# Kernel tuning notes

Measured on AMD Instinct MI355X. Metric: run time of the kernel, lower is better.

## Reference

```python
import jax, jax.numpy as jnp
import numpy as np

B, S, F, H = 16, 2048, 1024, 16
D = F // H
EPS = 1e-5


def setup_inputs() -> dict:
    key = jax.random.key(0)
    ks = jax.random.split(key, 10)
    scale = 1.0 / np.sqrt(F)
    return {
        "x": jax.random.normal(ks[0], (B, S, F), jnp.float32),
        "Wq": jax.random.normal(ks[1], (F, F), jnp.float32) * scale,
        "bq": jnp.zeros((F,), jnp.float32),
        "Wk": jax.random.normal(ks[2], (F, F), jnp.float32) * scale,
        "bk": jnp.zeros((F,), jnp.float32),
        "Wv": jax.random.normal(ks[3], (F, F), jnp.float32) * scale,
        "bv": jnp.zeros((F,), jnp.float32),
        "Wo": jax.random.normal(ks[4], (F, F), jnp.float32) * scale,
        "bo": jnp.zeros((F,), jnp.float32),
        "gamma": jnp.ones((F,), jnp.float32),
        "beta": jnp.zeros((F,), jnp.float32),
    }


def reference(x, Wq, bq, Wk, bk, Wv, bv, Wo, bo, gamma, beta):
    # x: (B, S, F). Dropout is identity in eval mode.
    b, s, f = x.shape
    q = (x @ Wq + bq).reshape(b, s, H, D)
    k = (x @ Wk + bk).reshape(b, s, H, D)
    v = (x @ Wv + bv).reshape(b, s, H, D)
    # Faithful to source: the einsum (applied to permuted tensors) contracts
    # across HEADS at each sequence position -> scores (B, S, H, H).
    energy = jnp.einsum('bshd,bsgd->bshg', q, k) / (D ** 0.5)
    attn = jax.nn.softmax(energy, axis=-1)  # softmax over key-head axis
    out = jnp.einsum('bshg,bsgd->bshd', attn, v).reshape(b, s, f)
    out = out @ Wo + bo
    # LayerNorm over last dim (eps=1e-5, affine)
    mu = jnp.mean(out, axis=-1, keepdims=True)
    var = jnp.mean((out - mu) ** 2, axis=-1, keepdims=True)
    return (out - mu) * jax.lax.rsqrt(var + EPS) * gamma + beta
```

## Files before the change

### kernel.cpp

```cpp
#include <hip/hip_runtime.h>
#include <hip/hip_bf16.h>
#include <stdint.h>

#define MM   32768
#define FFD  1024
#define NQKV 3072

typedef __bf16 bf16x8 __attribute__((ext_vector_type(8)));
typedef float  f32x4  __attribute__((ext_vector_type(4)));

__device__ __forceinline__ unsigned short f2bf_bits(float f){
  __hip_bfloat16 h = __float2bfloat16(f);
  unsigned short u;
  __builtin_memcpy(&u, &h, 2);
  return u;
}

__device__ __forceinline__ void gld16(const void* g, void* l){
  const unsigned int* gu = (const unsigned int*)g;
  unsigned int* lu = (unsigned int*)l;
  __builtin_amdgcn_global_load_lds(
      (const __attribute__((address_space(1))) unsigned int*)gu,
      (__attribute__((address_space(3))) unsigned int*)lu,
      16, 0, 0);
}

#define BARRIER() do { asm volatile("" ::: "memory"); \
                       __builtin_amdgcn_s_barrier();  \
                       asm volatile("" ::: "memory"); } while(0)

__global__ __launch_bounds__(256) void k_convert_bf16(const float* __restrict__ in,
                                                      unsigned short* __restrict__ out,
                                                      int n4){
  int i = blockIdx.x * 256 + threadIdx.x;
  if (i >= n4) return;
  float4 v = ((const float4*)in)[i];
  ushort4 r;
  r.x = f2bf_bits(v.x); r.y = f2bf_bits(v.y);
  r.z = f2bf_bits(v.z); r.w = f2bf_bits(v.w);
  ((ushort4*)out)[i] = r;
}

__global__ __launch_bounds__(256) void k_transpose_bf16(const float* __restrict__ in,
                                                        unsigned short* __restrict__ out,
                                                        int rows, int cols){
  __shared__ float tile[32][33];
  int bc = blockIdx.x * 32, br = blockIdx.y * 32;
  int tx = threadIdx.x, ty = threadIdx.y;
  #pragma unroll
  for (int j = 0; j < 32; j += 8)
    tile[ty + j][tx] = in[(size_t)(br + ty + j) * cols + bc + tx];
  __syncthreads();
  #pragma unroll
  for (int j = 0; j < 32; j += 8)
    out[(size_t)(bc + ty + j) * rows + br + tx] = f2bf_bits(tile[tx][ty + j]);
}

template <bool BF16OUT>
__global__ __launch_bounds__(512, 2) void k_gemm_bt(
    const unsigned short* __restrict__ A,
    const unsigned short* __restrict__ Bt,
    const float* __restrict__ b0, const float* __restrict__ b1, const float* __restrict__ b2,
    void* __restrict__ Cout, int M, int N, int K)
{
  __shared__ alignas(16) char smem[131072];

  const int tid  = threadIdx.x;
  const int lane = tid & 63;
  const int wave = tid >> 6;
  const int wr = wave >> 2, wc = wave & 3;
  const int quad = lane >> 4, lrow = lane & 15;
  const int sa = ((lrow >> 1) & 3) << 4;

  const int nwgx = gridDim.x;
  int nwg = nwgx * gridDim.y;
  int bid = blockIdx.y * nwgx + blockIdx.x;
  int cpx = nwg >> 3;
  int nid = (bid & 7) * cpx + (bid >> 3);
  int by = nid / nwgx;
  int bx = nid - by * nwgx;

  const long rowBase = (long)by * 256;
  const long colBase = (long)bx * 256;

  f32x4 acc[8][4];
  #pragma unroll
  for (int i = 0; i < 8; i++)
    #pragma unroll
    for (int j = 0; j < 4; j++)
      acc[i][j] = (f32x4){0.f, 0.f, 0.f, 0.f};

  const int swz8 = 8 * ((tid & 3) ^ ((tid >> 3) & 3));
  const unsigned short* gA = A  + (rowBase + (tid >> 2)) * (long)K + swz8;
  const unsigned short* gB = Bt + (colBase + (tid >> 2)) * (long)K + swz8;
  const long hstep = 128L * K;

  const int nk = K >> 5;

  #pragma unroll
  for (int tt = 0; tt < 3; ++tt){
    char* nb = smem + tt * 32768;
    gld16(gA + tt * 32,         nb +         tid * 16);
    gld16(gA + tt * 32 + hstep, nb +  8192 + tid * 16);
    gld16(gB + tt * 32,         nb + 16384 + tid * 16);
    gld16(gB + tt * 32 + hstep, nb + 24576 + tid * 16);
  }
  asm volatile("s_waitcnt vmcnt(8)" ::: "memory");
  BARRIER();

  for (int t = 0; t < nk; ++t){
    char* buf = smem + (t & 3) * 32768;
    char* nb  = smem + ((t + 3) & 3) * 32768;
    const unsigned short* sA = gA + (long)(t + 3) * 32;
    const unsigned short* sB = gB + (long)(t + 3) * 32;
    const bool st = (t < nk - 3);

    bf16x8 bfr[4];
    #pragma unroll
    for (int p = 0; p < 2; ++p){
      bf16x8 af[4];
      const char* ab = buf + wr * 8192 + p * 4096 + lrow * 64 + ((quad * 16) ^ sa);
      #pragma unroll
      for (int f = 0; f < 4; ++f)
        af[f] = *(const bf16x8*)(ab + f * 1024);
      if (p == 0){
        const char* bb = buf + 16384 + wc * 4096 + lrow * 64 + ((quad * 16) ^ sa);
        #pragma unroll
        for (int n = 0; n < 4; ++n)
          bfr[n] = *(const bf16x8*)(bb + n * 1024);
        if (st){
          gld16(sA,         nb +        tid * 16);
          gld16(sA + hstep, nb + 8192 + tid * 16);
        }
      } else {
        if (st){
          gld16(sB,         nb + 16384 + tid * 16);
          gld16(sB + hstep, nb + 24576 + tid * 16);
        }
      }
      BARRIER();
      __builtin_amdgcn_s_setprio(1);
      #pragma unroll
      for (int f = 0; f < 4; ++f)
        #pragma unroll
        for (int n = 0; n < 4; ++n)
          acc[p * 4 + f][n] =
              __builtin_amdgcn_mfma_f32_16x16x32_bf16(af[f], bfr[n], acc[p * 4 + f][n], 0, 0, 0);
      __builtin_amdgcn_s_setprio(0);
      if (p == 1){
        if (st)               asm volatile("s_waitcnt vmcnt(8)" ::: "memory");
        else if (t == nk - 3) asm volatile("s_waitcnt vmcnt(4)" ::: "memory");
        else if (t == nk - 2) asm volatile("s_waitcnt vmcnt(0)" ::: "memory");
      }
      BARRIER();
    }
  }

  #pragma unroll
  for (int n = 0; n < 4; ++n){
    long col = colBase + wc * 64 + n * 16 + lrow;
    const float* bp = (col < 1024) ? b0 : ((col < 2048) ? b1 : b2);
    float bias = bp[col & 1023];
    #pragma unroll
    for (int m = 0; m < 8; ++m){
      long row0 = rowBase + wr * 128 + (m >> 2) * 64 + (m & 3) * 16 + quad * 4;
      #pragma unroll
      for (int r = 0; r < 4; ++r){
        float v = acc[m][n][r] + bias;
        if constexpr (BF16OUT)
          ((unsigned short*)Cout)[(row0 + r) * (long)N + col] = f2bf_bits(v);
        else
          ((float*)Cout)[(row0 + r) * (long)N + col] = v;
      }
    }
  }
}

__global__ __launch_bounds__(256) void k_attention(const unsigned short* __restrict__ qkv,
                                                   unsigned short* __restrict__ aout){
  constexpr int QOFF = 0;
  constexpr int KOFF = 1152;
  constexpr int VOFF = 2304;
  constexpr int POFF = 4864;
  constexpr int PER  = 5504;
  __shared__ unsigned short smem[4 * PER];

  const int lane = threadIdx.x & 63;
  const int wave = threadIdx.x >> 6;
  const int pos  = blockIdx.x * 4 + wave;
  const int quad = lane >> 4, lidx = lane & 15;

  unsigned short* base = smem + wave * PER;
  unsigned short* Qb = base + QOFF;
  unsigned short* Kb = base + KOFF;
  unsigned short* Vt = base + VOFF;
  unsigned short* Pb = base + POFF;

  {
    uint4 z = {0u, 0u, 0u, 0u};
    *(uint4*)(Vt + lane * 40 + 16) = z;
    *(uint4*)(Vt + lane * 40 + 24) = z;
    *(uint2*)(Pb + (lane >> 2) * 40 + 16 + (lane & 3) * 4) = make_uint2(0u, 0u);
  }

  const unsigned short* src = qkv + (size_t)pos * 3072;
  #pragma unroll
  for (int i = 0; i < 6; i++){
    int c = i * 64 + lane;
    uint4 u = *(const uint4*)(src + c * 8);
    if (i < 4){
      unsigned short* mb = (c < 128) ? Qb : Kb;
      int cc = c & 127;
      *(uint4*)(mb + (cc >> 3) * 72 + (cc & 7) * 8) = u;
    } else {
      int cv = c - 256;
      int g = cv >> 3, d0 = (cv & 7) * 8;
      const unsigned short* us = (const unsigned short*)&u;
      #pragma unroll
      for (int t = 0; t < 8; t++) Vt[(d0 + t) * 40 + g] = us[t];
    }
  }
  __syncthreads();

  f32x4 s = (f32x4){0.f, 0.f, 0.f, 0.f};
  #pragma unroll
  for (int kk = 0; kk < 2; kk++){
    bf16x8 a = *(const bf16x8*)(Qb + lidx * 72 + kk * 32 + quad * 8);
    bf16x8 b = *(const bf16x8*)(Kb + lidx * 72 + kk * 32 + quad * 8);
    s = __builtin_amdgcn_mfma_f32_16x16x32_bf16(a, b, s, 0, 0, 0);
  }

  #pragma unroll
  for (int r = 0; r < 4; r++){
    float v = s[r] * 0.125f;
    float m = v;
    m = fmaxf(m, __shfl_xor(m, 1));
    m = fmaxf(m, __shfl_xor(m, 2));
    m = fmaxf(m, __shfl_xor(m, 4));
    m = fmaxf(m, __shfl_xor(m, 8));
    float e = __expf(v - m);
    float sum = e;
    sum += __shfl_xor(sum, 1);
    sum += __shfl_xor(sum, 2);
    sum += __shfl_xor(sum, 4);
    sum += __shfl_xor(sum, 8);
    float p = e / sum;
    Pb[(quad * 4 + r) * 40 + lidx] = f2bf_bits(p);
  }
  __syncthreads();

  f32x4 o[4];
  #pragma unroll
  for (int n4 = 0; n4 < 4; n4++){
    bf16x8 a = *(const bf16x8*)(Pb + lidx * 40 + quad * 8);
    bf16x8 b = *(const bf16x8*)(Vt + (n4 * 16 + lidx) * 40 + quad * 8);
    o[n4] = __builtin_amdgcn_mfma_f32_16x16x32_bf16(a, b, (f32x4){0.f,0.f,0.f,0.f}, 0, 0, 0);
  }

  #pragma unroll
  for (int n4 = 0; n4 < 4; n4++)
    #pragma unroll
    for (int r = 0; r < 4; r++)
      Qb[(quad * 4 + r) * 72 + n4 * 16 + lidx] = f2bf_bits(o[n4][r]);
  __syncthreads();

  unsigned short* dst = aout + (size_t)pos * 1024;
  #pragma unroll
  for (int t = 0; t < 2; t++){
    int j = lane * 2 + t;
    int h = j >> 3, dc = j & 7;
    uint4 u = *(const uint4*)(Qb + h * 72 + dc * 8);
    *(uint4*)(dst + j * 8) = u;
  }
}

__global__ __launch_bounds__(256) void k_ln(float* __restrict__ out,
                                            const float* __restrict__ gamma,
                                            const float* __restrict__ beta){
  __shared__ float red[8];
  int tid = threadIdx.x;
  float4* rowp = (float4*)(out + (size_t)blockIdx.x * 1024);
  float4 v = rowp[tid];
  float s  = v.x + v.y + v.z + v.w;
  float ss = v.x * v.x + v.y * v.y + v.z * v.z + v.w * v.w;
  #pragma unroll
  for (int off = 32; off > 0; off >>= 1){
    s  += __shfl_down(s, off);
    ss += __shfl_down(ss, off);
  }
  if ((tid & 63) == 0){ red[tid >> 6] = s; red[4 + (tid >> 6)] = ss; }
  __syncthreads();
  float S  = red[0] + red[1] + red[2] + red[3];
  float SS = red[4] + red[5] + red[6] + red[7];
  float mean = S * (1.0f / 1024.0f);
  float var  = SS * (1.0f / 1024.0f) - mean * mean;
  float rstd = rsqrtf(var + 1e-5f);
  float4 g = ((const float4*)gamma)[tid];
  float4 b = ((const float4*)beta)[tid];
  v.x = (v.x - mean) * rstd * g.x + b.x;
  v.y = (v.y - mean) * rstd * g.y + b.y;
  v.z = (v.z - mean) * rstd * g.z + b.z;
  v.w = (v.w - mean) * rstd * g.w + b.w;
  rowp[tid] = v;
}

extern "C" void kernel_launch(void* const* d_in, const int* in_sizes, int n_in,
                              void* d_out, int out_size, void* d_ws, size_t ws_size,
                              hipStream_t stream){
  const float* x     = (const float*)d_in[0];
  const float* Wq    = (const float*)d_in[1];
  const float* bq    = (const float*)d_in[2];
  const float* Wk    = (const float*)d_in[3];
  const float* bk    = (const float*)d_in[4];
  const float* Wv    = (const float*)d_in[5];
  const float* bv    = (const float*)d_in[6];
  const float* Wo    = (const float*)d_in[7];
  const float* bo    = (const float*)d_in[8];
  const float* gamma = (const float*)d_in[9];
  const float* beta  = (const float*)d_in[10];
  float* out = (float*)d_out;

  char* ws = (char*)d_ws;
  unsigned short* Wqkv_t = (unsigned short*)ws;
  unsigned short* Wo_t   = (unsigned short*)(ws + 6291456);
  unsigned short* xb     = (unsigned short*)(ws + 8388608);
  unsigned short* qkv    = (unsigned short*)(ws + 75497472);
  unsigned short* aout   = xb;

  k_convert_bf16<<<32768, 256, 0, stream>>>(x, xb, (MM * FFD) / 4);

  dim3 tb(32, 8), tg(32, 32);
  k_transpose_bf16<<<tg, tb, 0, stream>>>(Wq, Wqkv_t,                1024, 1024);
  k_transpose_bf16<<<tg, tb, 0, stream>>>(Wk, Wqkv_t + 1024 * 1024,  1024, 1024);
  k_transpose_bf16<<<tg, tb, 0, stream>>>(Wv, Wqkv_t + 2048 * 1024,  1024, 1024);
  k_transpose_bf16<<<tg, tb, 0, stream>>>(Wo, Wo_t,                  1024, 1024);

  k_gemm_bt<true><<<dim3(NQKV / 256, MM / 256), 512, 0, stream>>>(
      xb, Wqkv_t, bq, bk, bv, qkv, MM, NQKV, FFD);

  k_attention<<<MM / 4, 256, 0, stream>>>(qkv, aout);

  k_gemm_bt<false><<<dim3(FFD / 256, MM / 256), 512, 0, stream>>>(
      aout, Wo_t, bo, bo, bo, out, MM, FFD, FFD);

  k_ln<<<MM, 256, 0, stream>>>(out, gamma, beta);
}
```

Baseline: 655.3 us.

## Use one barrier per k-step in GEMM pipeline and stage bf16 epilogue through LDS

The GEMM main loop now waits on outstanding loads and syncs once at the top of each k-step, issues all four prefetch loads together, and hoists the B-fragment loads, where before it used two barriers per step with interleaved prefetches. For bf16 output the epilogue writes the tile to swizzled LDS and then does coalesced 16-byte global stores, replacing scattered 2-byte stores. This cuts barrier overhead and makes the QKV output writes efficient. It risks ring-buffer hazards, because the prefetch into slot t+3 is issued right after the barrier while other waves may still be reading that slot from step t-1. It also uses a non-ASCII identifier.

After: 631.0 us. 3.7% less time.

```diff
diff --git a/kernel.cpp b/kernel.cpp
--- a/kernel.cpp
+++ b/kernel.cpp
@@ -105,17 +105,30 @@
     gld16(gB + tt * 32,         nb + 16384 + tid * 16);
     gld16(gB + tt * 32 + hstep, nb + 24576 + tid * 16);
   }
-  asm volatile("s_waitcnt vmcnt(8)" ::: "memory");
-  BARRIER();
 
   for (int t = 0; t < nk; ++t){
+    if (t <= nk - 3)      asm volatile("s_waitcnt vmcnt(8)" ::: "memory");
+    else if (t == nk - 2) asm volatile("s_waitcnt vmcnt(4)" ::: "memory");
+    else                  asm volatile("s_waitcnt vmcnt(0)" ::: "memory");
+    BARRIER();
+
     char* buf = smem + (t & 3) * 32768;
-    char* nb  = smem + ((t + 3) & 3) * 32768;
-    const unsigned short* sA = gA + (long)(t + 3) * 32;
-    const unsigned short* sB = gB + (long)(t + 3) * 32;
-    const bool st = (t < nk - 3);
+    if (t < nk - 3){
+      char* nb = smem + ((t + 3) & 3) * 32768;
+      const unsigned short* sA = gA + (long)(t + 3) * 32;
+      const unsigned short* sB = gB + (long)(t + 3) * 32;
+      gld16(sA,         nb +         tid * 16);
+      gld16(sA + hstep, nb +  8192 + tid * 16);
+      gld16(sB,         nb + 16384 + tid * 16);
+      gld16(sB + 24576 / 16 * 0 + hstep, nb + 24576 + tid * 16);
+    }
 
     bf16x8 bfr[4];
+    const char* bb = buf + 16384 + wc * 4096 + lrow * 64 + ((quad * 16) ^ sa);
+    #pragma unroll
+    for (int n = 0; n < 4; ++n)
+      bfr[n] = *(const bf16x8*)(bb + n * 1024);
+
     #pragma unroll
     for (int p = 0; p < 2; ++p){
       bf16x8 af[4];
@@ -123,22 +136,6 @@
       #pragma unroll
       for (int f = 0; f < 4; ++f)
         af[f] = *(const bf16x8*)(ab + f * 1024);
-      if (p == 0){
-        const char* bb = buf + 16384 + wc * 4096 + lrow * 64 + ((quad * 16) ^ sa);
-        #pragma unroll
-        for (int n = 0; n < 4; ++n)
-          bfr[n] = *(const bf16x8*)(bb + n * 1024);
-        if (st){
-          gld16(sA,         nb +        tid * 16);
-          gld16(sA + hstep, nb + 8192 + tid * 16);
-        }
-      } else {
-        if (st){
-          gld16(sB,         nb + 16384 + tid * 16);
-          gld16(sB + hstep, nb + 24576 + tid * 16);
-        }
-      }
-      BARRIER();
       __builtin_amdgcn_s_setprio(1);
       #pragma unroll
       for (int f = 0; f < 4; ++f)
@@ -147,30 +144,54 @@
           acc[p * 4 + f][n] =
               __builtin_amdgcn_mfma_f32_16x16x32_bf16(af[f], bfr[n], acc[p * 4 + f][n], 0, 0, 0);
       __builtin_amdgcn_s_setprio(0);
-      if (p == 1){
-        if (st)               asm volatile("s_waitcnt vmcnt(8)" ::: "memory");
-        else if (t == nk - 3) asm volatile("s_waitcnt vmcnt(4)" ::: "memory");
-        else if (t == nk - 2) asm volatile("s_waitcnt vmcnt(0)" ::: "memory");
+    }
+  }
+
+  if constexpr (BF16OUT){
+    BARRIER();
+    #pragma unroll
+    for (int n = 0; n < 4; ++n){
+      int lcol = wc * 64 + n * 16 + lrow;
+      long col = colBase + lcol;
+      const float* bp = (col < 1024) ? b0 : ((col < 2048) ? b1 : b2);
+      float bias = bp[col & 1023];
+      #pragma unroll
+      for (int m = 0; m < 8; ++m){
+        int row0 = wr * 128 + (m >> 2) * 64 + (m & 3) * 16 + quad * 4;
+        int sw = ((row0 >> 2) & 3) << 5;
+        #pragma unroll
+        for (int r = 0; r < 4; ++r){
+          float v = acc[m][n][r] + bias;
+          int byte = (row0 + r) * 512 + ((lcol * 2) ^ sw);
+          *(unsigned short*)(smem + byte) = f2bf_bits(v);
+        }
       }
-      BARRIER();
-    }
-  }
-
-  #pragma unroll
-  for (int n = 0; n < 4; ++n){
-    long col = colBase + wc * 64 + n * 16 + lrow;
-    const float* bp = (col < 1024) ? b0 : ((col < 2048) ? b1 : b2);
-    float bias = bp[col & 1023];
-    #pragma unroll
-    for (int m = 0; m < 8; ++m){
-      long row0 = rowBase + wr * 128 + (m >> 2) * 64 + (m & 3) * 16 + quad * 4;
-      #pragma unroll
-      for (int r = 0; r < 4; ++r){
-        float v = acc[m][n][r] + bias;
-        if constexpr (BF16OUT)
-          ((unsigned short*)Cout)[(row0 + r) * (long)N + col] = f2bf_bits(v);
-        else
+    }
+    asm volatile("s_waitcnt lgkmcnt(0)" ::: "memory");
+    BARRIER();
+    unsigned short* Cо = (unsigned short*)Cout;
+    #pragma unroll
+    for (int i = 0; i < 16; ++i){
+      int c = i * 512 + tid;
+      int row = c >> 5, cidx = c & 31;
+      int rb = (cidx ^ (((row >> 2) & 3) << 1)) * 16;
+      uint4 u = *(const uint4*)(smem + row * 512 + rb);
+      *(uint4*)(Cо + (rowBase + row) * (long)N + colBase + cidx * 8) = u;
+    }
+  } else {
+    #pragma unroll
+    for (int n = 0; n < 4; ++n){
+      long col = colBase + wc * 64 + n * 16 + lrow;
+      const float* bp = (col < 1024) ? b0 : ((col < 2048) ? b1 : b2);
+      float bias = bp[col & 1023];
+      #pragma unroll
+      for (int m = 0; m < 8; ++m){
+        long row0 = rowBase + wr * 128 + (m >> 2) * 64 + (m & 3) * 16 + quad * 4;
+        #pragma unroll
+        for (int r = 0; r < 4; ++r){
+          float v = acc[m][n][r] + bias;
           ((float*)Cout)[(row0 + r) * (long)N + col] = v;
+        }
       }
     }
   }
```
